# Kernel optimization log

Measured on AMD Instinct MI355X. Metric: run time of the kernel, lower is better.

## Reference

```python
import jax, jax.numpy as jnp
import numpy as np

K = 5  # k_neighbors


def _pairwise_sq(a, b):
    # (B,N,3),(B,M,3) -> (B,N,M) squared euclidean distances (matmul form)
    d = (jnp.sum(a * a, -1)[:, :, None] + jnp.sum(b * b, -1)[:, None, :]
         - 2.0 * jnp.einsum('bnd,bmd->bnm', a, b))
    return jnp.maximum(d, 0.0)


def _knn_indices(points, k):
    # (B,N,3) -> (B,N,k) indices of k nearest neighbors, excluding self
    d = _pairwise_sq(points, points)
    _, idx = jax.lax.top_k(-d, k + 1)
    return idx[:, :, 1:]


def _gather_neighbors(feats, idx):
    # feats (B,N,C), idx (B,N,k) -> (B,N,k,C)
    B, N, k = idx.shape
    flat = jnp.take_along_axis(feats, idx.reshape(B, N * k, 1), axis=1)
    return flat.reshape(B, N, k, feats.shape[-1])


def setup_inputs() -> dict:
    key = jax.random.key(0)
    ks = jax.random.split(key, 8)
    B, N, M = 8, 4096, 4000
    return {
        'Y': jax.random.normal(ks[0], (B, N, 3), jnp.float32),
        'X': jax.random.normal(ks[1], (B, M, 3), jnp.float32),
        'R_pred': jax.random.normal(ks[2], (B, 3, 3), jnp.float32),
        't_pred': jax.random.normal(ks[3], (B, 3), jnp.float32),
        'R_gt': jax.random.normal(ks[4], (B, 3, 3), jnp.float32),
        't_gt': jax.random.normal(ks[5], (B, 3), jnp.float32),
        'X_hat': jax.random.normal(ks[6], (B, N, 3), jnp.float32),
        'delta': jax.random.normal(ks[7], (B, N, 3), jnp.float32),
    }


def reference(Y, X, R_pred, t_pred, R_gt, t_gt, X_hat, delta):
    lam_rot, lam_trans, lam_rmse = 1.0, 1.0, 1.0
    lam_align, lam_disp, lam_deform, lam_lap = 1.0, 0.01, 0.1, 0.1

    # --- rigid losses ---
    # rotation geodesic: R_delta = R_pred^T @ R_gt
    R_delta = jnp.einsum('bij,bik->bjk', R_pred, R_gt)
    tr = jnp.trace(R_delta, axis1=1, axis2=2)
    cos_a = jnp.clip((tr - 1.0) / 2.0, -1.0 + 1e-7, 1.0 - 1e-7)
    L_rot = jnp.mean(jnp.arccos(cos_a))

    L_trans = jnp.mean(jnp.linalg.norm(t_pred - t_gt, axis=1))

    # Y @ R^T + t
    Y_pred = jnp.einsum('bnd,bkd->bnk', Y, R_pred) + t_pred[:, None, :]
    Y_gt = jnp.einsum('bnd,bkd->bnk', Y, R_gt) + t_gt[:, None, :]
    L_rmse = jnp.mean(jnp.sqrt(jnp.mean(jnp.sum((Y_pred - Y_gt) ** 2, -1), axis=1)))

    rigid = lam_rot * L_rot + lam_trans * L_trans + lam_rmse * L_rmse

    # --- non-rigid losses ---
    Y_rigid = Y_pred  # apply_rigid_transform(Y, R_pred, t_pred)

    # alignment: N != M -> kNN matching of X_hat against X
    d_align = _pairwise_sq(X_hat, X)          # (B,N,M)
    knn_d = -jax.lax.top_k(-d_align, K)[0]    # (B,N,K) smallest distances
    L_align = jnp.mean(knn_d)

    L_disp = jnp.mean(jnp.sum(delta ** 2, -1))

    # kNN graph on Y_rigid (original builds it twice with identical result)
    idx = _knn_indices(Y_rigid, K)            # (B,N,K)

    Yn = _gather_neighbors(Y_rigid, idx)      # (B,N,K,3)
    Xn = _gather_neighbors(X_hat, idx)
    edge_diff = (Xn - X_hat[:, :, None, :]) - (Yn - Y_rigid[:, :, None, :])
    L_deform = jnp.mean(jnp.sum(edge_diff ** 2, -1))

    dn = _gather_neighbors(delta, idx)        # (B,N,K,3)
    lap = delta - jnp.mean(dn, axis=2)
    L_lap = jnp.mean(jnp.sum(lap ** 2, -1))

    non_rigid = (lam_align * L_align + lam_disp * L_disp
                 + lam_deform * L_deform + lam_lap * L_lap)
    total = rigid + non_rigid

    return jnp.stack([total, rigid, non_rigid, L_rot, L_trans, L_rmse,
                      L_align, L_disp, L_deform, L_lap])
```

## Files before the change

### kernel.cpp

```cpp
#include <hip/hip_runtime.h>
#include <math.h>

#define BB 8
#define NN 4096
#define MM 4000
#define KK 5
#define NWAVE 8
#define QPB 64
#define CH 512
#define NPAD 4096
#define SCAN_BLOCKS ((NN / QPB) * BB * 2)

#define ACC_ROT    0
#define ACC_TRANS  1
#define ACC_ALIGN  2
#define ACC_DISP   3
#define ACC_DEFORM 4
#define ACC_LAP    5
#define ACC_RMSE   6
#define ACC_COUNT  14

#define INFF __int_as_float(0x7F800000)

__device__ __forceinline__ float waveReduceSum(float v) {
#pragma unroll
    for (int off = 32; off > 0; off >>= 1) v += __shfl_down(v, off, 64);
    return v;
}

template<bool SELF, bool PACK>
__device__ __forceinline__ void proc1(float4 c, int midx, int q,
                                      float ca, float cbq, float cc,
                                      float& b0, float& b1, float& b2,
                                      float& b3, float& b4) {
    float sc = fmaf(c.x, ca, fmaf(c.y, cbq, fmaf(c.z, cc, c.w)));
    float v;
    if (PACK) {
        unsigned pk = (__float_as_uint(sc) & 0xFFFFF000u) | (unsigned)midx;
        v = __uint_as_float(pk);
        if (SELF) v = (midx == q) ? INFF : v;
    } else {
        v = sc;
    }
    float n0 = fminf(b0, v);
    float n1 = __builtin_amdgcn_fmed3f(v, b0, b1);
    float n2 = __builtin_amdgcn_fmed3f(v, b1, b2);
    float n3 = __builtin_amdgcn_fmed3f(v, b2, b3);
    float n4 = __builtin_amdgcn_fmed3f(v, b3, b4);
    b0 = n0; b1 = n1; b2 = n2; b3 = n3; b4 = n4;
}

template<bool SELF, bool PACK>
__device__ __forceinline__ void scanLDS(const float4* __restrict__ lc, int tc,
                                        float ca, float cbq, float cc, int q,
                                        float& b0, float& b1, float& b2,
                                        float& b3, float& b4) {
    float4 A[8], B[8];
#pragma unroll
    for (int j = 0; j < 8; ++j) A[j] = lc[tc + j];

    for (int t0 = 0; t0 < CH; t0 += 16) {
#pragma unroll
        for (int j = 0; j < 8; ++j) B[j] = lc[tc + t0 + 8 + j];
#pragma unroll
        for (int j = 0; j < 8; ++j)
            proc1<SELF, PACK>(A[j], tc + t0 + j, q, ca, cbq, cc, b0, b1, b2, b3, b4);
        if (t0 + 16 < CH) {
#pragma unroll
            for (int j = 0; j < 8; ++j) A[j] = lc[tc + t0 + 16 + j];
        }
#pragma unroll
        for (int j = 0; j < 8; ++j)
            proc1<SELF, PACK>(B[j], tc + t0 + 8 + j, q, ca, cbq, cc, b0, b1, b2, b3, b4);
    }
}

__global__ void k_prep(const float* __restrict__ Y, const float* __restrict__ X,
                       const float* __restrict__ Rp, const float* __restrict__ tp,
                       const float* __restrict__ Rg, const float* __restrict__ tg,
                       const float* __restrict__ dl,
                       float4* __restrict__ YrP, float4* __restrict__ XP,
                       float* __restrict__ acc) {
    int b = blockIdx.x >> 4;
    int n = ((blockIdx.x & 15) << 8) + threadIdx.x;
    size_t base = ((size_t)b * NN + n) * 3;
    float yx = Y[base + 0], yy = Y[base + 1], yz = Y[base + 2];

    float rp[9], rg[9], tpv[3], tgv[3];
#pragma unroll
    for (int i = 0; i < 9; ++i) { rp[i] = Rp[b * 9 + i]; rg[i] = Rg[b * 9 + i]; }
#pragma unroll
    for (int i = 0; i < 3; ++i) { tpv[i] = tp[b * 3 + i]; tgv[i] = tg[b * 3 + i]; }

    float p[3], dr2 = 0.f;
#pragma unroll
    for (int k = 0; k < 3; ++k) {
        float pv = fmaf(yx, rp[k * 3 + 0], fmaf(yy, rp[k * 3 + 1], fmaf(yz, rp[k * 3 + 2], tpv[k])));
        float gv = fmaf(yx, rg[k * 3 + 0], fmaf(yy, rg[k * 3 + 1], fmaf(yz, rg[k * 3 + 2], tgv[k])));
        p[k] = pv;
        float dd = pv - gv;
        dr2 = fmaf(dd, dd, dr2);
    }
    YrP[(size_t)b * NPAD + n] =
        make_float4(p[0], p[1], p[2], fmaf(p[0], p[0], fmaf(p[1], p[1], p[2] * p[2])));

    float4 xe;
    if (n < MM) {
        size_t xb = ((size_t)b * MM + n) * 3;
        float x0 = X[xb + 0], x1 = X[xb + 1], x2 = X[xb + 2];
        xe = make_float4(x0, x1, x2, fmaf(x0, x0, fmaf(x1, x1, x2 * x2)));
    } else {
        xe = make_float4(0.f, 0.f, 0.f, INFF);
    }
    XP[(size_t)b * NPAD + n] = xe;

    float d0 = dl[base + 0], d1 = dl[base + 1], d2 = dl[base + 2];
    float dsq = d0 * d0 + d1 * d1 + d2 * d2;

    dr2 = waveReduceSum(dr2);
    dsq = waveReduceSum(dsq);
    if ((threadIdx.x & 63) == 0) {
        atomicAdd(&acc[ACC_RMSE + b], dr2);
        atomicAdd(&acc[ACC_DISP], dsq);
    }

    if (threadIdx.x == 0 && (blockIdx.x & 15) == 0) {
        float tr = 0.f;
#pragma unroll
        for (int i = 0; i < 9; ++i) tr += rp[i] * rg[i];
        float c = (tr - 1.f) * 0.5f;
        c = fminf(fmaxf(c, -1.f + 1e-7f), 1.f - 1e-7f);
        float dx = tpv[0] - tgv[0], dy = tpv[1] - tgv[1], dz = tpv[2] - tgv[2];
        atomicAdd(&acc[ACC_ROT], acosf(c));
        atomicAdd(&acc[ACC_TRANS], sqrtf(dx * dx + dy * dy + dz * dz));
    }
}

__device__ void finalize(const float* acc, float* out) {
    float a[ACC_COUNT];
#pragma unroll
    for (int i = 0; i < ACC_COUNT; ++i)
        a[i] = __hip_atomic_load(&acc[i], __ATOMIC_RELAXED, __HIP_MEMORY_SCOPE_AGENT);
    float L_rot = a[ACC_ROT] / BB;
    float L_trans = a[ACC_TRANS] / BB;
    float L_rmse = 0.f;
#pragma unroll
    for (int b = 0; b < BB; ++b) L_rmse += sqrtf(a[ACC_RMSE + b] / NN);
    L_rmse /= BB;
    float L_align = a[ACC_ALIGN] / ((float)BB * NN * KK);
    float L_disp = a[ACC_DISP] / ((float)BB * NN);
    float L_def = a[ACC_DEFORM] / ((float)BB * NN * KK);
    float L_lap = a[ACC_LAP] / ((float)BB * NN);
    float rigid = L_rot + L_trans + L_rmse;
    float nr = L_align + 0.01f * L_disp + 0.1f * L_def + 0.1f * L_lap;
    out[0] = rigid + nr; out[1] = rigid; out[2] = nr;
    out[3] = L_rot; out[4] = L_trans; out[5] = L_rmse;
    out[6] = L_align; out[7] = L_disp; out[8] = L_def; out[9] = L_lap;
}

#define MERGE_STEP(W) { float d = md[W][l][pp##W]; if (d < best) { best = d; bw = W; } }
#define MERGE_ADV()  { pp0 += (bw == 0); pp1 += (bw == 1); pp2 += (bw == 2); pp3 += (bw == 3); \
                       pp4 += (bw == 4); pp5 += (bw == 5); pp6 += (bw == 6); pp7 += (bw == 7); }

__global__ __launch_bounds__(512, 4) void k_scan(const float* __restrict__ Xh,
                                                 const float4* __restrict__ XP,
                                                 const float4* __restrict__ YrP,
                                                 const float* __restrict__ dl,
                                                 float* __restrict__ acc,
                                                 unsigned* __restrict__ doneCnt,
                                                 float* __restrict__ out) {
    __shared__ float4 lc[NPAD];
    __shared__ float md[NWAVE][QPB][6];
    int tid = threadIdx.x, wave = tid >> 6, lane = tid & 63;
    int qg = blockIdx.x, b = blockIdx.y, mode = blockIdx.z;
    int q = qg * QPB + lane;

    const float4* cbG = (mode == 0 ? XP : YrP) + (size_t)b * NPAD;
#pragma unroll
    for (int i = 0; i < NPAD / 512; ++i) lc[tid + i * 512] = cbG[tid + i * 512];

    float qx, qy, qz, qn = 0.f;
    float4 qp;
    if (mode == 0) {
        size_t a0 = ((size_t)b * NN + q) * 3;
        qx = Xh[a0 + 0]; qy = Xh[a0 + 1]; qz = Xh[a0 + 2];
        qn = fmaf(qx, qx, fmaf(qy, qy, qz * qz));
    } else {
        qp = cbG[q];
        qx = qp.x; qy = qp.y; qz = qp.z;
    }
    __syncthreads();

    float b0 = INFF, b1 = INFF, b2 = INFF, b3 = INFF, b4 = INFF;
    int tc = wave * CH;
    if (mode == 0) {
        scanLDS<false, false>(lc, tc, -2.f * qx, -2.f * qy, -2.f * qz, 0,
                              b0, b1, b2, b3, b4);
    } else if (wave == (qg >> 3)) {
        scanLDS<true, true>(lc, tc, -2.f * qx, -2.f * qy, -2.f * qz, q,
                            b0, b1, b2, b3, b4);
    } else {
        scanLDS<false, true>(lc, tc, -2.f * qx, -2.f * qy, -2.f * qz, q,
                             b0, b1, b2, b3, b4);
    }

    md[wave][lane][0] = b0; md[wave][lane][1] = b1; md[wave][lane][2] = b2;
    md[wave][lane][3] = b3; md[wave][lane][4] = b4; md[wave][lane][5] = INFF;
    __syncthreads();

    if (tid < QPB) {
        int l = tid;
        int pp0 = 0, pp1 = 0, pp2 = 0, pp3 = 0, pp4 = 0, pp5 = 0, pp6 = 0, pp7 = 0;
        if (mode == 0) {
            float s = 0.f;
#pragma unroll
            for (int k = 0; k < KK; ++k) {
                float best = INFF; int bw = 0;
                MERGE_STEP(0) MERGE_STEP(1) MERGE_STEP(2) MERGE_STEP(3)
                MERGE_STEP(4) MERGE_STEP(5) MERGE_STEP(6) MERGE_STEP(7)
                s += fmaxf(best + qn, 0.f);
                MERGE_ADV()
            }
            s = waveReduceSum(s);
            if (l == 0) atomicAdd(&acc[ACC_ALIGN], s);
        } else {
            int si[KK];
#pragma unroll
            for (int k = 0; k < KK; ++k) {
                float best = INFF; int bw = 0;
                MERGE_STEP(0) MERGE_STEP(1) MERGE_STEP(2) MERGE_STEP(3)
                MERGE_STEP(4) MERGE_STEP(5) MERGE_STEP(6) MERGE_STEP(7)
                si[k] = (int)(__float_as_uint(best) & 0xFFFu);
                MERGE_ADV()
            }
            const float* xh = Xh + (size_t)b * NN * 3;
            const float* dlb = dl + (size_t)b * NN * 3;
            float xnx = xh[q * 3 + 0], xny = xh[q * 3 + 1], xnz = xh[q * 3 + 2];
            float dnx = dlb[q * 3 + 0], dny = dlb[q * 3 + 1], dnz = dlb[q * 3 + 2];

            float def = 0.f, sx = 0.f, sy = 0.f, sz = 0.f;
#pragma unroll
            for (int k = 0; k < KK; ++k) {
                int n = si[k];
                float4 yj = lc[n];
                float ex = (xh[n * 3 + 0] - xnx) - (yj.x - qp.x);
                float ey = (xh[n * 3 + 1] - xny) - (yj.y - qp.y);
                float ez = (xh[n * 3 + 2] - xnz) - (yj.z - qp.z);
                def += ex * ex + ey * ey + ez * ez;
                sx += dlb[n * 3 + 0]; sy += dlb[n * 3 + 1]; sz += dlb[n * 3 + 2];
            }
            float lx = dnx - sx / 5.f, ly = dny - sy / 5.f, lz = dnz - sz / 5.f;
            float lap = lx * lx + ly * ly + lz * lz;

            def = waveReduceSum(def);
            lap = waveReduceSum(lap);
            if (l == 0) {
                atomicAdd(&acc[ACC_DEFORM], def);
                atomicAdd(&acc[ACC_LAP], lap);
            }
        }
    }
    __syncthreads();
    if (tid == 0) {
        __threadfence();
        unsigned t = __hip_atomic_fetch_add(doneCnt, 1u, __ATOMIC_ACQ_REL,
                                            __HIP_MEMORY_SCOPE_AGENT);
        if (t == SCAN_BLOCKS - 1) finalize(acc, out);
    }
}

extern "C" void kernel_launch(void* const* d_in, const int* in_sizes, int n_in,
                              void* d_out, int out_size, void* d_ws, size_t ws_size,
                              hipStream_t stream) {
    const float* Y  = (const float*)d_in[0];
    const float* X  = (const float*)d_in[1];
    const float* Rp = (const float*)d_in[2];
    const float* tp = (const float*)d_in[3];
    const float* Rg = (const float*)d_in[4];
    const float* tg = (const float*)d_in[5];
    const float* Xh = (const float*)d_in[6];
    const float* dl = (const float*)d_in[7];
    float* out = (float*)d_out;

    float*    acc     = (float*)d_ws;
    unsigned* doneCnt = (unsigned*)((char*)d_ws + 64);
    float4*   YrP     = (float4*)((char*)d_ws + 512);
    float4*   XP      = YrP + (size_t)BB * NPAD;

    hipMemsetAsync(d_ws, 0, 512, stream);
    hipLaunchKernelGGL(k_prep, dim3(BB * NN / 256), dim3(256), 0, stream,
                       Y, X, Rp, tp, Rg, tg, dl, YrP, XP, acc);
    hipLaunchKernelGGL(k_scan, dim3(NN / QPB, BB, 2), dim3(512), 0, stream,
                       Xh, XP, YrP, dl, acc, doneCnt, out);
}
```

Measured before the change: 111.5 us.

## Broadcast candidate points via readlane from registers instead of LDS staging

Removes the per-block copy of the whole candidate set into LDS and the barrier after it. Each wave now loads 64 candidates per tile from global memory, one per lane, and broadcasts them with readlane (scalar registers), prefetching the next tile. The smaller LDS footprint lets the launch bounds rise to 8 blocks per CU. The cost is extra scalar readlane instructions per candidate and repeated global/L2 reads, and the neighbor gather now reads from global memory.

```diff
diff --git a/kernel.cpp b/kernel.cpp
--- a/kernel.cpp
+++ b/kernel.cpp
@@ -8,6 +8,7 @@
 #define NWAVE 8
 #define QPB 64
 #define CH 512
+#define NTILE (CH / 64)
 #define NPAD 4096
 #define SCAN_BLOCKS ((NN / QPB) * BB * 2)
 
@@ -28,50 +29,42 @@
     return v;
 }
 
+__device__ __forceinline__ float rlane(float v, int l) {
+    return __int_as_float(__builtin_amdgcn_readlane(__float_as_int(v), l));
+}
+
 template<bool SELF, bool PACK>
-__device__ __forceinline__ void proc1(float4 c, int midx, int q,
-                                      float ca, float cbq, float cc,
-                                      float& b0, float& b1, float& b2,
-                                      float& b3, float& b4) {
-    float sc = fmaf(c.x, ca, fmaf(c.y, cbq, fmaf(c.z, cc, c.w)));
-    float v;
-    if (PACK) {
-        unsigned pk = (__float_as_uint(sc) & 0xFFFFF000u) | (unsigned)midx;
-        v = __uint_as_float(pk);
-        if (SELF) v = (midx == q) ? INFF : v;
-    } else {
-        v = sc;
-    }
-    float n0 = fminf(b0, v);
-    float n1 = __builtin_amdgcn_fmed3f(v, b0, b1);
-    float n2 = __builtin_amdgcn_fmed3f(v, b1, b2);
-    float n3 = __builtin_amdgcn_fmed3f(v, b2, b3);
-    float n4 = __builtin_amdgcn_fmed3f(v, b3, b4);
-    b0 = n0; b1 = n1; b2 = n2; b3 = n3; b4 = n4;
-}
-
-template<bool SELF, bool PACK>
-__device__ __forceinline__ void scanLDS(const float4* __restrict__ lc, int tc,
+__device__ __forceinline__ void scanReg(const float4* __restrict__ cb, int tc,
                                         float ca, float cbq, float cc, int q,
+                                        int lane,
                                         float& b0, float& b1, float& b2,
                                         float& b3, float& b4) {
-    float4 A[8], B[8];
-#pragma unroll
-    for (int j = 0; j < 8; ++j) A[j] = lc[tc + j];
-
-    for (int t0 = 0; t0 < CH; t0 += 16) {
-#pragma unroll
-        for (int j = 0; j < 8; ++j) B[j] = lc[tc + t0 + 8 + j];
-#pragma unroll
-        for (int j = 0; j < 8; ++j)
-            proc1<SELF, PACK>(A[j], tc + t0 + j, q, ca, cbq, cc, b0, b1, b2, b3, b4);
-        if (t0 + 16 < CH) {
-#pragma unroll
-            for (int j = 0; j < 8; ++j) A[j] = lc[tc + t0 + 16 + j];
+    float4 cur = cb[tc + lane];
+    for (int t = 0; t < NTILE; ++t) {
+        float4 nxt = cur;
+        if (t + 1 < NTILE) nxt = cb[tc + (t + 1) * 64 + lane];
+        int mbase = tc + t * 64;
+#pragma unroll
+        for (int j = 0; j < 64; ++j) {
+            float cx = rlane(cur.x, j), cy = rlane(cur.y, j);
+            float cz = rlane(cur.z, j), cw = rlane(cur.w, j);
+            float sc = fmaf(cx, ca, fmaf(cy, cbq, cz * cc + cw));
+            float v;
+            if (PACK) {
+                unsigned pk = (__float_as_uint(sc) & 0xFFFFF000u) | (unsigned)(mbase + j);
+                v = __uint_as_float(pk);
+                if (SELF) v = (mbase + j == q) ? INFF : v;
+            } else {
+                v = sc;
+            }
+            float n0 = fminf(b0, v);
+            float n1 = __builtin_amdgcn_fmed3f(v, b0, b1);
+            float n2 = __builtin_amdgcn_fmed3f(v, b1, b2);
+            float n3 = __builtin_amdgcn_fmed3f(v, b2, b3);
+            float n4 = __builtin_amdgcn_fmed3f(v, b3, b4);
+            b0 = n0; b1 = n1; b2 = n2; b3 = n3; b4 = n4;
         }
-#pragma unroll
-        for (int j = 0; j < 8; ++j)
-            proc1<SELF, PACK>(B[j], tc + t0 + 8 + j, q, ca, cbq, cc, b0, b1, b2, b3, b4);
+        cur = nxt;
     }
 }
 
@@ -162,22 +155,19 @@
 #define MERGE_ADV()  { pp0 += (bw == 0); pp1 += (bw == 1); pp2 += (bw == 2); pp3 += (bw == 3); \
                        pp4 += (bw == 4); pp5 += (bw == 5); pp6 += (bw == 6); pp7 += (bw == 7); }
 
-__global__ __launch_bounds__(512, 4) void k_scan(const float* __restrict__ Xh,
+__global__ __launch_bounds__(512, 8) void k_scan(const float* __restrict__ Xh,
                                                  const float4* __restrict__ XP,
                                                  const float4* __restrict__ YrP,
                                                  const float* __restrict__ dl,
                                                  float* __restrict__ acc,
                                                  unsigned* __restrict__ doneCnt,
                                                  float* __restrict__ out) {
-    __shared__ float4 lc[NPAD];
     __shared__ float md[NWAVE][QPB][6];
     int tid = threadIdx.x, wave = tid >> 6, lane = tid & 63;
     int qg = blockIdx.x, b = blockIdx.y, mode = blockIdx.z;
     int q = qg * QPB + lane;
 
     const float4* cbG = (mode == 0 ? XP : YrP) + (size_t)b * NPAD;
-#pragma unroll
-    for (int i = 0; i < NPAD / 512; ++i) lc[tid + i * 512] = cbG[tid + i * 512];
 
     float qx, qy, qz, qn = 0.f;
     float4 qp;
@@ -189,18 +179,17 @@
         qp = cbG[q];
         qx = qp.x; qy = qp.y; qz = qp.z;
     }
-    __syncthreads();
 
     float b0 = INFF, b1 = INFF, b2 = INFF, b3 = INFF, b4 = INFF;
     int tc = wave * CH;
     if (mode == 0) {
-        scanLDS<false, false>(lc, tc, -2.f * qx, -2.f * qy, -2.f * qz, 0,
+        scanReg<false, false>(cbG, tc, -2.f * qx, -2.f * qy, -2.f * qz, 0, lane,
                               b0, b1, b2, b3, b4);
     } else if (wave == (qg >> 3)) {
-        scanLDS<true, true>(lc, tc, -2.f * qx, -2.f * qy, -2.f * qz, q,
+        scanReg<true, true>(cbG, tc, -2.f * qx, -2.f * qy, -2.f * qz, q, lane,
                             b0, b1, b2, b3, b4);
     } else {
-        scanLDS<false, true>(lc, tc, -2.f * qx, -2.f * qy, -2.f * qz, q,
+        scanReg<false, true>(cbG, tc, -2.f * qx, -2.f * qy, -2.f * qz, q, lane,
                              b0, b1, b2, b3, b4);
     }
 
@@ -242,7 +231,7 @@
 #pragma unroll
             for (int k = 0; k < KK; ++k) {
                 int n = si[k];
-                float4 yj = lc[n];
+                float4 yj = cbG[n];
                 float ex = (xh[n * 3 + 0] - xnx) - (yj.x - qp.x);
                 float ey = (xh[n * 3 + 1] - xny) - (yj.y - qp.y);
                 float ez = (xh[n * 3 + 2] - xnz) - (yj.z - qp.z);
```

New measurement: 167.9 us. +50.6%, slower.
